# Kernel optimization log

Measured on AMD Instinct MI355X. Metric: run time of the kernel, lower is better.

The kernel has to match this reference:

```python
import jax, jax.numpy as jnp
import numpy as np

TOPK = 2048


def setup_inputs() -> dict:
    key = jax.random.key(0)
    ks = jax.random.split(key, 16)
    M = 20000
    boxes = jax.random.uniform(ks[0], (M, 4), dtype=jnp.float32)
    scores = jax.random.uniform(ks[1], (M,), dtype=jnp.float32)
    classes = jax.random.randint(ks[2], (M,), 0, 80, dtype=jnp.int64)
    def lin(k, fan_in, fan_out):
        b = 1.0 / np.sqrt(fan_in)
        kw, kb = jax.random.split(k)
        w = jax.random.uniform(kw, (fan_in, fan_out), jnp.float32, -b, b)
        bias = jax.random.uniform(kb, (fan_out,), jnp.float32, -b, b)
        return w, bias
    sup_w1, sup_b1 = lin(ks[3], 7, 32)
    sup_w2, sup_b2 = lin(ks[4], 32, 16)
    sup_w3, sup_b3 = lin(ks[5], 16, 1)
    lam_w1, lam_b1 = lin(ks[6], 5, 16)
    lam_w2, lam_b2 = lin(ks[7], 16, 1)
    return {
        'boxes': boxes, 'scores': scores, 'classes': classes,
        'sup_w1': sup_w1, 'sup_b1': sup_b1, 'sup_w2': sup_w2, 'sup_b2': sup_b2,
        'sup_w3': sup_w3, 'sup_b3': sup_b3,
        'lam_w1': lam_w1, 'lam_b1': lam_b1, 'lam_w2': lam_w2, 'lam_b2': lam_b2,
    }


def _box_iou(b):
    # b: [N,4] in (x, y, w, h)
    x, y, w, h = b[:, 0], b[:, 1], b[:, 2], b[:, 3]
    area = w * h
    ix1 = jnp.maximum(x[:, None], x[None, :])
    iy1 = jnp.maximum(y[:, None], y[None, :])
    ix2 = jnp.minimum((x + w)[:, None], (x + w)[None, :])
    iy2 = jnp.minimum((y + h)[:, None], (y + h)[None, :])
    inter = jnp.clip(ix2 - ix1, 0) * jnp.clip(iy2 - iy1, 0)
    union = area[:, None] + area[None, :] - inter
    return inter / (union + 1e-06)


def _dacs(boxes, scores, classes,
          sup_w1, sup_b1, sup_w2, sup_b2, sup_w3, sup_b3,
          lam_w1, lam_b1, lam_w2, lam_b2):
    k = min(TOPK, scores.shape[0])
    top_scores, idx = jax.lax.top_k(scores, k)
    b = boxes[idx]            # [N,4]
    cls = classes[idx]        # [N]
    N = k
    iou = _box_iou(b)         # [N,N]
    D = iou.mean(axis=1)      # [N]
    x, y, w, h = b[:, 0], b[:, 1], b[:, 2], b[:, 3]
    feats = jnp.stack([
        iou,
        jnp.abs(x[:, None] - x[None, :]),
        jnp.abs(y[:, None] - y[None, :]),
        jnp.abs(w[:, None] - w[None, :]),
        jnp.abs(h[:, None] - h[None, :]),
        jnp.broadcast_to(top_scores[:, None], (N, N)),
        jnp.broadcast_to(top_scores[None, :], (N, N)),
    ], axis=-1)               # [N,N,7]
    hdn = jax.nn.relu(feats @ sup_w1 + sup_b1)       # [N,N,32]
    hdn = jax.nn.relu(hdn @ sup_w2 + sup_b2)         # [N,N,16]
    s_ij = jax.nn.sigmoid((hdn @ sup_w3 + sup_b3)[..., 0])  # [N,N]
    class_mask = (cls[:, None] == cls[None, :]).astype(s_ij.dtype)
    s_ij = s_ij * class_mask
    lam_in = jnp.concatenate([b, top_scores[:, None]], axis=1)  # [N,5]
    lam_h = jax.nn.relu(lam_in @ lam_w1 + lam_b1)
    lam = jax.nn.sigmoid((lam_h @ lam_w2 + lam_b2)[:, 0])       # [N]
    S = jnp.sum(s_ij * iou, axis=1)
    E = lam * S * D
    new_scores = top_scores * jnp.exp(-E)
    return b, new_scores, cls


def reference(boxes, scores, classes,
              sup_w1, sup_b1, sup_w2, sup_b2, sup_w3, sup_b3,
              lam_w1, lam_b1, lam_w2, lam_b2):
    return _dacs(boxes, scores, classes,
                 sup_w1, sup_b1, sup_w2, sup_b2, sup_w3, sup_b3,
                 lam_w1, lam_b1, lam_w2, lam_b2)
```

## Files before the change

kernel.cpp:

```cpp
#include <hip/hip_runtime.h>
#include <math.h>

#define TOPK 2048
#define NCLS 80
#define NBIN 4096
#define CMAX 2560
#define TN   1024
#define CROWS 8

struct P {
    const float* scores; const float* boxes; const int* classes;
    const float* sw1; const float* sb1; const float* sw2; const float* sb2;
    const float* sw3; const float* sb3;
    const float* lw1; const float* lb1; const float* lw2; const float* lb2;
    int M; int K;
    float* out_boxes; float* out_scores; float* out_cls;
};

__device__ __forceinline__ float iou_of(float xi, float yi, float ai,
                                        float x2i, float y2i, float4 bj) {
    float ix1 = fmaxf(xi, bj.x), iy1 = fmaxf(yi, bj.y);
    float ix2 = fminf(x2i, bj.x + bj.z), iy2 = fminf(y2i, bj.y + bj.w);
    float iw = fmaxf(ix2 - ix1, 0.0f), ih = fmaxf(iy2 - iy1, 0.0f);
    float inter = iw * ih;
    float uni = ai + bj.z * bj.w - inter;
    return inter / (uni + 1e-6f);
}

__device__ __forceinline__ int digest12(float s) {
    int v = (int)(s * 4096.0f);
    return v < 0 ? 0 : (v > NBIN - 1 ? NBIN - 1 : v);
}

__device__ __forceinline__ float key_score(unsigned long long kk) {
    unsigned mono = (unsigned)(kk >> 32);
    unsigned ob = (mono & 0x80000000u) ? (mono & 0x7FFFFFFFu) : ~mono;
    return __uint_as_float(ob);
}

__global__ __launch_bounds__(TN, 1) void k_dacs(P p) {
    __shared__ int   bincur[NBIN];
    __shared__ int   binbase[NBIN];
    __shared__ unsigned long long skeys[CMAX];
    __shared__ int   sfx[TN];
    __shared__ int   wsum[TN / 64];
    __shared__ int   sh_cT;
    __shared__ float4 sbox[TOPK];
    __shared__ float  sscore[TOPK];
    __shared__ short  scls[TOPK];
    __shared__ short  clist[TOPK];
    __shared__ int    ccnt[NCLS], ccur[NCLS], cstart[NCLS + 1];
    __shared__ int    wtot;
    __shared__ float  swt[914];
    __shared__ float  wpart[TN / 64];
    __shared__ int    rowc[CROWS];
    __shared__ int    prefix[CROWS + 1];
    __shared__ float  Ssum[CROWS], Drow[CROWS];

    int tid = threadIdx.x, bid = blockIdx.x;
    int M = p.M, K = p.K, M4 = M >> 2;
    int r0 = bid * CROWS;
    int nrows = K - r0; if (nrows > CROWS) nrows = CROWS;
    if (nrows <= 0) return;

    for (int t = tid; t < 224; t += TN) swt[t] = p.sw1[t];
    if (tid < 32) swt[224 + tid] = p.sb1[tid];
    for (int t = tid; t < 512; t += TN) swt[256 + t] = p.sw2[t];
    if (tid < 16) swt[768 + tid] = p.sb2[tid];
    if (tid < 16) swt[784 + tid] = p.sw3[tid];
    if (tid == 0) swt[800] = p.sb3[0];
    if (tid < 80) swt[801 + tid] = p.lw1[tid];
    if (tid < 16) swt[881 + tid] = p.lb1[tid];
    if (tid < 16) swt[897 + tid] = p.lw2[tid];
    if (tid == 0) swt[913] = p.lb2[0];

    for (int b = tid; b < NBIN; b += TN) bincur[b] = 0;
    if (tid < NCLS) ccnt[tid] = 0;
    if (tid < CROWS) Ssum[tid] = 0.0f;
    __syncthreads();

    const float4* s4p = (const float4*)p.scores;
    for (int i4 = tid; i4 < M4; i4 += TN) {
        float4 v = s4p[i4];
        atomicAdd(&bincur[digest12(v.x)], 1);
        atomicAdd(&bincur[digest12(v.y)], 1);
        atomicAdd(&bincur[digest12(v.z)], 1);
        atomicAdd(&bincur[digest12(v.w)], 1);
    }
    for (int i = M4 * 4 + tid; i < M; i += TN)
        atomicAdd(&bincur[digest12(p.scores[i])], 1);
    __syncthreads();

    {
        const int BPT = NBIN / TN;
        int c0 = tid * BPT, sum = 0;
        #pragma unroll
        for (int u = 0; u < BPT; u++) sum += bincur[c0 + u];
        int lane = tid & 63;
        int x = sum;
        #pragma unroll
        for (int off = 1; off < 64; off <<= 1) {
            int v = __shfl_down(x, off, 64);
            if (lane + off < 64) x += v;
        }
        if (lane == 0) wsum[tid >> 6] = x;
        __syncthreads();
        if (tid < TN / 64) {
            int t = wsum[tid];
            #pragma unroll
            for (int off = 1; off < TN / 64; off <<= 1) {
                int v = __shfl_down(t, off, 64);
                if (tid + off < TN / 64) t += v;
            }
            wsum[tid] = t;
        }
        __syncthreads();
        int wid = tid >> 6;
        int higher = (wid < TN / 64 - 1) ? wsum[wid + 1] : 0;
        sfx[tid] = x + higher;
    }
    __syncthreads();

    {
        const int BPT = NBIN / TN;
        int running = (tid < TN - 1) ? sfx[tid + 1] : 0;
        int c0 = tid * BPT;
        for (int u = BPT - 1; u >= 0; u--) {
            int b = c0 + u, cnt = bincur[b];
            binbase[b] = running;
            if (running < K && running + cnt >= K) sh_cT = b;
            running += cnt;
        }
    }
    __syncthreads();
    int cT = sh_cT;
    for (int b = tid; b < NBIN; b += TN) bincur[b] = binbase[b];
    __syncthreads();

    for (int i4 = tid; i4 < M4; i4 += TN) {
        float4 v = s4p[i4];
        #pragma unroll
        for (int u = 0; u < 4; u++) {
            float s = (u == 0) ? v.x : (u == 1) ? v.y : (u == 2) ? v.z : v.w;
            int d = digest12(s);
            if (d >= cT) {
                int i = i4 * 4 + u;
                int slot = atomicAdd(&bincur[d], 1);
                if (slot < CMAX) {
                    unsigned b = __float_as_uint(s);
                    b = (b & 0x80000000u) ? ~b : (b | 0x80000000u);
                    skeys[slot] = ((unsigned long long)b << 32) |
                                  (unsigned long long)(0xFFFFFFFFu - (unsigned)i);
                }
            }
        }
    }
    for (int i = M4 * 4 + tid; i < M; i += TN) {
        float s = p.scores[i];
        int d = digest12(s);
        if (d >= cT) {
            int slot = atomicAdd(&bincur[d], 1);
            if (slot < CMAX) {
                unsigned b = __float_as_uint(s);
                b = (b & 0x80000000u) ? ~b : (b | 0x80000000u);
                skeys[slot] = ((unsigned long long)b << 32) |
                              (unsigned long long)(0xFFFFFFFFu - (unsigned)i);
            }
        }
    }
    __syncthreads();

    int C = bincur[cT]; if (C > CMAX) C = CMAX;
    {
        const float4* boxes4 = (const float4*)p.boxes;
        for (int s = tid; s < C; s += TN) {
            unsigned long long ks = skeys[s];
            unsigned idx = 0xFFFFFFFFu - (unsigned)(ks & 0xFFFFFFFFull);
            float sc = key_score(ks);
            int d = digest12(sc);
            int st = binbase[d], en = bincur[d]; if (en > CMAX) en = CMAX;
            int r = binbase[d];
            for (int t = st; t < en; t++) r += (skeys[t] > ks) ? 1 : 0;
            if (r < K) {
                sbox[r] = boxes4[idx];
                sscore[r] = sc;
                scls[r] = (short)p.classes[idx];
            }
        }
    }
    __syncthreads();

    for (int r = tid; r < K; r += TN) atomicAdd(&ccnt[scls[r]], 1);
    __syncthreads();
    {
        int x = 0, v = 0;
        if (tid < 128) {
            v = (tid < NCLS) ? ccnt[tid] : 0;
            x = v;
            #pragma unroll
            for (int off = 1; off < 64; off <<= 1) {
                int t = __shfl_up(x, off, 64);
                if ((tid & 63) >= off) x += t;
            }
            if (tid == 63) wtot = x;
        }
        __syncthreads();
        if (tid < NCLS) {
            int excl = x - v + ((tid >= 64) ? wtot : 0);
            ccur[tid] = excl;
            cstart[tid] = excl;
        }
        if (tid == 0) cstart[NCLS] = K;
        __syncthreads();
        for (int r = tid; r < K; r += TN) {
            int pos = atomicAdd(&ccur[scls[r]], 1);
            clist[pos] = (short)r;
        }
    }
    __syncthreads();

    {
        int wv = tid >> 6, lane = tid & 63;
        int row = wv >> 1, half = wv & 1;
        float dsum = 0.0f;
        if (row < nrows) {
            float4 bi = sbox[r0 + row];
            float ai = bi.z * bi.w, x2i = bi.x + bi.z, y2i = bi.y + bi.w;
            for (int j = lane + (half << 6); j < K; j += 128)
                dsum += iou_of(bi.x, bi.y, ai, x2i, y2i, sbox[j]);
            #pragma unroll
            for (int off = 32; off >= 1; off >>= 1)
                dsum += __shfl_xor(dsum, off, 64);
        }
        if (lane == 0) wpart[wv] = dsum;
    }

    if (tid < CROWS) {
        int st = 0, cnt = 0;
        if (tid < nrows) {
            int c = scls[r0 + tid];
            st = cstart[c];
            cnt = cstart[c + 1] - st;
        }
        rowc[tid] = st;
        prefix[tid] = cnt;
    }
    __syncthreads();
    if (tid < nrows) Drow[tid] = (wpart[2 * tid] + wpart[2 * tid + 1]) / (float)K;
    if (tid == 0) {
        int acc = 0;
        #pragma unroll
        for (int rr = 0; rr < CROWS; rr++) { int t = prefix[rr]; prefix[rr] = acc; acc += t; }
        prefix[CROWS] = acc;
    }
    __syncthreads();

    int Pb = prefix[CROWS];
    const float* W1 = swt;       const float* B1 = swt + 224;
    const float* W2 = swt + 256; const float* B2 = swt + 768;
    const float* W3 = swt + 784; float B3 = swt[800];

    for (int pp = tid; pp < Pb; pp += TN) {
        int lo = 0, hi = CROWS;
        while (hi - lo > 1) {
            int mid = (lo + hi) >> 1;
            if (prefix[mid] <= pp) lo = mid; else hi = mid;
        }
        int row = lo;
        int j = (int)clist[rowc[row] + (pp - prefix[row])];
        float4 bi = sbox[r0 + row];
        float4 bj = sbox[j];
        float ai = bi.z * bi.w, x2i = bi.x + bi.z, y2i = bi.y + bi.w;
        float iou = iou_of(bi.x, bi.y, ai, x2i, y2i, bj);
        float f1 = fabsf(bi.x - bj.x), f2 = fabsf(bi.y - bj.y);
        float f3 = fabsf(bi.z - bj.z), f4 = fabsf(bi.w - bj.w);
        float f5 = sscore[r0 + row], f6 = sscore[j];
        float acc2[16];
        #pragma unroll
        for (int q = 0; q < 16; q++) acc2[q] = B2[q];
        #pragma unroll 2
        for (int o = 0; o < 32; o++) {
            float a = B1[o];
            a += iou * W1[0 * 32 + o];
            a += f1 * W1[1 * 32 + o];
            a += f2 * W1[2 * 32 + o];
            a += f3 * W1[3 * 32 + o];
            a += f4 * W1[4 * 32 + o];
            a += f5 * W1[5 * 32 + o];
            a += f6 * W1[6 * 32 + o];
            float h = fmaxf(a, 0.0f);
            #pragma unroll
            for (int q = 0; q < 16; q++) acc2[q] += h * W2[o * 16 + q];
        }
        float acc3 = B3;
        #pragma unroll
        for (int q = 0; q < 16; q++) acc3 += fmaxf(acc2[q], 0.0f) * W3[q];
        atomicAdd(&Ssum[row], iou / (1.0f + expf(-acc3)));
    }
    __syncthreads();

    if (tid < nrows) {
        int r = r0 + tid;
        float4 bi = sbox[r];
        float si = sscore[r];
        const float* LW1 = swt + 801; const float* LB1 = swt + 881;
        const float* LW2 = swt + 897; float LB2 = swt[913];
        float in5[5] = { bi.x, bi.y, bi.z, bi.w, si };
        float acc = LB2;
        #pragma unroll
        for (int o = 0; o < 16; o++) {
            float a2 = LB1[o];
            #pragma unroll
            for (int f = 0; f < 5; f++) a2 += in5[f] * LW1[f * 16 + o];
            acc += fmaxf(a2, 0.0f) * LW2[o];
        }
        float lam = 1.0f / (1.0f + expf(-acc));
        ((float4*)p.out_boxes)[r] = bi;
        p.out_cls[r] = (float)scls[r];
        p.out_scores[r] = si * expf(-lam * Ssum[tid] * Drow[tid]);
    }
}

extern "C" void kernel_launch(void* const* d_in, const int* in_sizes, int n_in,
                              void* d_out, int out_size, void* d_ws, size_t ws_size,
                              hipStream_t stream) {
    int M = in_sizes[1];
    int K = (M < TOPK) ? M : TOPK;

    P dp;
    dp.scores  = (const float*)d_in[1];
    dp.boxes   = (const float*)d_in[0];
    dp.classes = (const int*)d_in[2];
    dp.sw1 = (const float*)d_in[3];  dp.sb1 = (const float*)d_in[4];
    dp.sw2 = (const float*)d_in[5];  dp.sb2 = (const float*)d_in[6];
    dp.sw3 = (const float*)d_in[7];  dp.sb3 = (const float*)d_in[8];
    dp.lw1 = (const float*)d_in[9];  dp.lb1 = (const float*)d_in[10];
    dp.lw2 = (const float*)d_in[11]; dp.lb2 = (const float*)d_in[12];
    dp.M = M; dp.K = K;
    dp.out_boxes  = (float*)d_out;
    dp.out_scores = (float*)d_out + (size_t)K * 4;
    dp.out_cls    = (float*)d_out + (size_t)K * 5;

    int nb = (K + CROWS - 1) / CROWS;
    k_dacs<<<nb, TN, 0, stream>>>(dp);
}
```

Before: 102.9 us.

## Split monolithic kernel into single-pass top-k selection plus pairwise compute kernels

Result: slower. 106.9 us (+3.9%).

```diff
diff --git a/kernel.cpp b/kernel.cpp
--- a/kernel.cpp
+++ b/kernel.cpp
@@ -5,17 +5,23 @@
 #define NCLS 80
 #define NBIN 4096
 #define CMAX 2560
-#define TN   1024
-#define CROWS 8
-
-struct P {
-    const float* scores; const float* boxes; const int* classes;
-    const float* sw1; const float* sb1; const float* sw2; const float* sb2;
-    const float* sw3; const float* sb3;
-    const float* lw1; const float* lb1; const float* lw2; const float* lb2;
-    int M; int K;
-    float* out_boxes; float* out_scores; float* out_cls;
-};
+#define TNA  1024
+#define TND  512
+#define CROWS 4
+
+
+struct SelAP { const float* scores; int M; int K; int* ghist; int* gmeta; };
+struct ScatP { const float* scores; int M; int* ghist; const int* gmeta;
+               unsigned long long* gskeys; };
+struct RankP { const float* boxes; const int* classes; const int* ghist;
+               const int* gmeta; const unsigned long long* gskeys; int K;
+               float4* selB; float* selS; int* selC; };
+struct CmpP  { const float4* selB; const float* selS; const int* selC;
+               const float* sw1; const float* sb1; const float* sw2; const float* sb2;
+               const float* sw3; const float* sb3;
+               const float* lw1; const float* lb1; const float* lw2; const float* lb2;
+               int K;
+               float* out_boxes; float* out_scores; float* out_cls; };
 
 __device__ __forceinline__ float iou_of(float xi, float yi, float ai,
                                         float x2i, float y2i, float4 bj) {
@@ -32,40 +38,159 @@
     return v < 0 ? 0 : (v > NBIN - 1 ? NBIN - 1 : v);
 }
 
+__device__ __forceinline__ unsigned long long make_key(float s, unsigned i) {
+    unsigned b = __float_as_uint(s);
+    b = (b & 0x80000000u) ? ~b : (b | 0x80000000u);
+    return ((unsigned long long)b << 32) |
+           (unsigned long long)(0xFFFFFFFFu - i);
+}
+
 __device__ __forceinline__ float key_score(unsigned long long kk) {
     unsigned mono = (unsigned)(kk >> 32);
     unsigned ob = (mono & 0x80000000u) ? (mono & 0x7FFFFFFFu) : ~mono;
     return __uint_as_float(ob);
 }
 
-__global__ __launch_bounds__(TN, 1) void k_dacs(P p) {
-    __shared__ int   bincur[NBIN];
-    __shared__ int   binbase[NBIN];
-    __shared__ unsigned long long skeys[CMAX];
-    __shared__ int   sfx[TN];
-    __shared__ int   wsum[TN / 64];
-    __shared__ int   sh_cT;
-    __shared__ float4 sbox[TOPK];
-    __shared__ float  sscore[TOPK];
-    __shared__ short  scls[TOPK];
-    __shared__ short  clist[TOPK];
-    __shared__ int    ccnt[NCLS], ccur[NCLS], cstart[NCLS + 1];
-    __shared__ int    wtot;
-    __shared__ float  swt[914];
-    __shared__ float  wpart[TN / 64];
-    __shared__ int    rowc[CROWS];
-    __shared__ int    prefix[CROWS + 1];
-    __shared__ float  Ssum[CROWS], Drow[CROWS];
+__global__ __launch_bounds__(TNA, 1) void k_selA(SelAP p) {
+    __shared__ int lbin[NBIN];
+    __shared__ int sfx[TNA];
+    __shared__ int wsum[TNA / 64];
+    __shared__ int sh_cT;
+
+    int tid = threadIdx.x;
+    int M = p.M, K = p.K, M4 = M >> 2;
+
+    for (int b = tid; b < NBIN; b += TNA) lbin[b] = 0;
+    __syncthreads();
+
+    const float4* s4p = (const float4*)p.scores;
+    for (int i4 = tid; i4 < M4; i4 += TNA) {
+        float4 v = s4p[i4];
+        atomicAdd(&lbin[digest12(v.x)], 1);
+        atomicAdd(&lbin[digest12(v.y)], 1);
+        atomicAdd(&lbin[digest12(v.z)], 1);
+        atomicAdd(&lbin[digest12(v.w)], 1);
+    }
+    for (int i = M4 * 4 + tid; i < M; i += TNA)
+        atomicAdd(&lbin[digest12(p.scores[i])], 1);
+    __syncthreads();
+
+    {
+        const int BPT = NBIN / TNA;
+        int c0 = tid * BPT, sum = 0;
+        #pragma unroll
+        for (int u = 0; u < BPT; u++) sum += lbin[c0 + u];
+        int lane = tid & 63;
+        int x = sum;
+        #pragma unroll
+        for (int off = 1; off < 64; off <<= 1) {
+            int v = __shfl_down(x, off, 64);
+            if (lane + off < 64) x += v;
+        }
+        if (lane == 0) wsum[tid >> 6] = x;
+        __syncthreads();
+        if (tid < TNA / 64) {
+            int t = wsum[tid];
+            #pragma unroll
+            for (int off = 1; off < TNA / 64; off <<= 1) {
+                int v = __shfl_down(t, off, 64);
+                if (tid + off < TNA / 64) t += v;
+            }
+            wsum[tid] = t;
+        }
+        __syncthreads();
+        int wid = tid >> 6;
+        int higher = (wid < TNA / 64 - 1) ? wsum[wid + 1] : 0;
+        sfx[tid] = x + higher;
+    }
+    __syncthreads();
+
+    {
+        const int BPT = NBIN / TNA;
+        int running = (tid < TNA - 1) ? sfx[tid + 1] : 0;
+        int c0 = tid * BPT;
+        for (int u = BPT - 1; u >= 0; u--) {
+            int b = c0 + u, cnt = lbin[b];
+            if (running < K && running + cnt >= K) sh_cT = b;
+            p.ghist[b] = (running << 16);
+            running += cnt;
+        }
+    }
+    __syncthreads();
+    if (tid == 0) p.gmeta[0] = sh_cT;
+}
+
+__global__ void k_scat(ScatP p) {
+    int nt = gridDim.x * blockDim.x;
+    int gt = blockIdx.x * blockDim.x + threadIdx.x;
+    int cT = p.gmeta[0];
+    int M = p.M, M4 = M >> 2;
+    const float4* s4p = (const float4*)p.scores;
+    for (int i4 = gt; i4 < M4; i4 += nt) {
+        float4 v = s4p[i4];
+        #pragma unroll
+        for (int u = 0; u < 4; u++) {
+            float s = (u == 0) ? v.x : (u == 1) ? v.y : (u == 2) ? v.z : v.w;
+            int d = digest12(s);
+            if (d >= cT) {
+                int old = atomicAdd(&p.ghist[d], 1);
+                int slot = (old >> 16) + (old & 0xFFFF);
+                if (slot < CMAX)
+                    p.gskeys[slot] = make_key(s, (unsigned)(i4 * 4 + u));
+            }
+        }
+    }
+    for (int i = M4 * 4 + gt; i < M; i += nt) {
+        float s = p.scores[i];
+        int d = digest12(s);
+        if (d >= cT) {
+            int old = atomicAdd(&p.ghist[d], 1);
+            int slot = (old >> 16) + (old & 0xFFFF);
+            if (slot < CMAX) p.gskeys[slot] = make_key(s, (unsigned)i);
+        }
+    }
+}
+
+__global__ void k_rank(RankP p) {
+    int t = blockIdx.x * blockDim.x + threadIdx.x;
+    int cT = p.gmeta[0];
+    int pkT = p.ghist[cT];
+    int C = (pkT >> 16) + (pkT & 0xFFFF); if (C > CMAX) C = CMAX;
+    if (t >= C) return;
+    unsigned long long ks = p.gskeys[t];
+    unsigned idx = 0xFFFFFFFFu - (unsigned)(ks & 0xFFFFFFFFull);
+    float sc = key_score(ks);
+    int d = digest12(sc);
+    int pk = p.ghist[d];
+    int st = pk >> 16;
+    int en = st + (pk & 0xFFFF); if (en > CMAX) en = CMAX;
+    int r = st;
+    for (int q = st; q < en; q++) r += (p.gskeys[q] > ks) ? 1 : 0;
+    if (r < p.K) {
+        p.selB[r] = ((const float4*)p.boxes)[idx];
+        p.selS[r] = sc;
+        p.selC[r] = p.classes[idx];
+    }
+}
+
+__global__ __launch_bounds__(TND, 2) void k_cmp(CmpP p) {
+    __shared__ float swt[914];
+    __shared__ short mlist[CROWS * TOPK];
+    __shared__ int   mcnt[CROWS];
+    __shared__ int   rowcls[CROWS];
+    __shared__ int   prefix[CROWS + 1];
+    __shared__ float wpart[TND / 64];
+    __shared__ float Ssum[CROWS], Drow[CROWS];
 
     int tid = threadIdx.x, bid = blockIdx.x;
-    int M = p.M, K = p.K, M4 = M >> 2;
+    int K = p.K;
     int r0 = bid * CROWS;
     int nrows = K - r0; if (nrows > CROWS) nrows = CROWS;
     if (nrows <= 0) return;
 
-    for (int t = tid; t < 224; t += TN) swt[t] = p.sw1[t];
+    for (int t = tid; t < 224; t += TND) swt[t] = p.sw1[t];
     if (tid < 32) swt[224 + tid] = p.sb1[tid];
-    for (int t = tid; t < 512; t += TN) swt[256 + t] = p.sw2[t];
+    for (int t = tid; t < 512; t += TND) swt[256 + t] = p.sw2[t];
     if (tid < 16) swt[768 + tid] = p.sb2[tid];
     if (tid < 16) swt[784 + tid] = p.sw3[tid];
     if (tid == 0) swt[800] = p.sb3[0];
@@ -74,183 +199,45 @@
     if (tid < 16) swt[897 + tid] = p.lw2[tid];
     if (tid == 0) swt[913] = p.lb2[0];
 
-    for (int b = tid; b < NBIN; b += TN) bincur[b] = 0;
-    if (tid < NCLS) ccnt[tid] = 0;
-    if (tid < CROWS) Ssum[tid] = 0.0f;
-    __syncthreads();
-
-    const float4* s4p = (const float4*)p.scores;
-    for (int i4 = tid; i4 < M4; i4 += TN) {
-        float4 v = s4p[i4];
-        atomicAdd(&bincur[digest12(v.x)], 1);
-        atomicAdd(&bincur[digest12(v.y)], 1);
-        atomicAdd(&bincur[digest12(v.z)], 1);
-        atomicAdd(&bincur[digest12(v.w)], 1);
-    }
-    for (int i = M4 * 4 + tid; i < M; i += TN)
-        atomicAdd(&bincur[digest12(p.scores[i])], 1);
-    __syncthreads();
-
-    {
-        const int BPT = NBIN / TN;
-        int c0 = tid * BPT, sum = 0;
-        #pragma unroll
-        for (int u = 0; u < BPT; u++) sum += bincur[c0 + u];
-        int lane = tid & 63;
-        int x = sum;
-        #pragma unroll
-        for (int off = 1; off < 64; off <<= 1) {
-            int v = __shfl_down(x, off, 64);
-            if (lane + off < 64) x += v;
-        }
-        if (lane == 0) wsum[tid >> 6] = x;
-        __syncthreads();
-        if (tid < TN / 64) {
-            int t = wsum[tid];
-            #pragma unroll
-            for (int off = 1; off < TN / 64; off <<= 1) {
-                int v = __shfl_down(t, off, 64);
-                if (tid + off < TN / 64) t += v;
+    if (tid < CROWS) {
+        mcnt[tid] = 0;
+        Ssum[tid] = 0.0f;
+        rowcls[tid] = (tid < nrows) ? p.selC[r0 + tid] : -1;
+    }
+    __syncthreads();
+
+    for (int j = tid; j < K; j += TND) {
+        int c = p.selC[j];
+        #pragma unroll
+        for (int rr = 0; rr < CROWS; rr++) {
+            if (c == rowcls[rr]) {
+                int pos = atomicAdd(&mcnt[rr], 1);
+                mlist[rr * TOPK + pos] = (short)j;
             }
-            wsum[tid] = t;
-        }
-        __syncthreads();
-        int wid = tid >> 6;
-        int higher = (wid < TN / 64 - 1) ? wsum[wid + 1] : 0;
-        sfx[tid] = x + higher;
-    }
-    __syncthreads();
-
-    {
-        const int BPT = NBIN / TN;
-        int running = (tid < TN - 1) ? sfx[tid + 1] : 0;
-        int c0 = tid * BPT;
-        for (int u = BPT - 1; u >= 0; u--) {
-            int b = c0 + u, cnt = bincur[b];
-            binbase[b] = running;
-            if (running < K && running + cnt >= K) sh_cT = b;
-            running += cnt;
-        }
-    }
-    __syncthreads();
-    int cT = sh_cT;
-    for (int b = tid; b < NBIN; b += TN) bincur[b] = binbase[b];
-    __syncthreads();
-
-    for (int i4 = tid; i4 < M4; i4 += TN) {
-        float4 v = s4p[i4];
-        #pragma unroll
-        for (int u = 0; u < 4; u++) {
-            float s = (u == 0) ? v.x : (u == 1) ? v.y : (u == 2) ? v.z : v.w;
-            int d = digest12(s);
-            if (d >= cT) {
-                int i = i4 * 4 + u;
-                int slot = atomicAdd(&bincur[d], 1);
-                if (slot < CMAX) {
-                    unsigned b = __float_as_uint(s);
-                    b = (b & 0x80000000u) ? ~b : (b | 0x80000000u);
-                    skeys[slot] = ((unsigned long long)b << 32) |
-                                  (unsigned long long)(0xFFFFFFFFu - (unsigned)i);
-                }
-            }
-        }
-    }
-    for (int i = M4 * 4 + tid; i < M; i += TN) {
-        float s = p.scores[i];
-        int d = digest12(s);
-        if (d >= cT) {
-            int slot = atomicAdd(&bincur[d], 1);
-            if (slot < CMAX) {
-                unsigned b = __float_as_uint(s);
-                b = (b & 0x80000000u) ? ~b : (b | 0x80000000u);
-                skeys[slot] = ((unsigned long long)b << 32) |
-                              (unsigned long long)(0xFFFFFFFFu - (unsigned)i);
-            }
-        }
-    }
-    __syncthreads();
-
-    int C = bincur[cT]; if (C > CMAX) C = CMAX;
-    {
-        const float4* boxes4 = (const float4*)p.boxes;
-        for (int s = tid; s < C; s += TN) {
-            unsigned long long ks = skeys[s];
-            unsigned idx = 0xFFFFFFFFu - (unsigned)(ks & 0xFFFFFFFFull);
-            float sc = key_score(ks);
-            int d = digest12(sc);
-            int st = binbase[d], en = bincur[d]; if (en > CMAX) en = CMAX;
-            int r = binbase[d];
-            for (int t = st; t < en; t++) r += (skeys[t] > ks) ? 1 : 0;
-            if (r < K) {
-                sbox[r] = boxes4[idx];
-                sscore[r] = sc;
-                scls[r] = (short)p.classes[idx];
-            }
-        }
-    }
-    __syncthreads();
-
-    for (int r = tid; r < K; r += TN) atomicAdd(&ccnt[scls[r]], 1);
-    __syncthreads();
-    {
-        int x = 0, v = 0;
-        if (tid < 128) {
-            v = (tid < NCLS) ? ccnt[tid] : 0;
-            x = v;
-            #pragma unroll
-            for (int off = 1; off < 64; off <<= 1) {
-                int t = __shfl_up(x, off, 64);
-                if ((tid & 63) >= off) x += t;
-            }
-            if (tid == 63) wtot = x;
-        }
-        __syncthreads();
-        if (tid < NCLS) {
-            int excl = x - v + ((tid >= 64) ? wtot : 0);
-            ccur[tid] = excl;
-            cstart[tid] = excl;
-        }
-        if (tid == 0) cstart[NCLS] = K;
-        __syncthreads();
-        for (int r = tid; r < K; r += TN) {
-            int pos = atomicAdd(&ccur[scls[r]], 1);
-            clist[pos] = (short)r;
-        }
-    }
-    __syncthreads();
+        }
+    }
 
     {
         int wv = tid >> 6, lane = tid & 63;
         int row = wv >> 1, half = wv & 1;
         float dsum = 0.0f;
         if (row < nrows) {
-            float4 bi = sbox[r0 + row];
+            float4 bi = p.selB[r0 + row];
             float ai = bi.z * bi.w, x2i = bi.x + bi.z, y2i = bi.y + bi.w;
             for (int j = lane + (half << 6); j < K; j += 128)
-                dsum += iou_of(bi.x, bi.y, ai, x2i, y2i, sbox[j]);
+                dsum += iou_of(bi.x, bi.y, ai, x2i, y2i, p.selB[j]);
             #pragma unroll
             for (int off = 32; off >= 1; off >>= 1)
                 dsum += __shfl_xor(dsum, off, 64);
         }
         if (lane == 0) wpart[wv] = dsum;
     }
-
-    if (tid < CROWS) {
-        int st = 0, cnt = 0;
-        if (tid < nrows) {
-            int c = scls[r0 + tid];
-            st = cstart[c];
-            cnt = cstart[c + 1] - st;
-        }
-        rowc[tid] = st;
-        prefix[tid] = cnt;
-    }
     __syncthreads();
     if (tid < nrows) Drow[tid] = (wpart[2 * tid] + wpart[2 * tid + 1]) / (float)K;
     if (tid == 0) {
         int acc = 0;
         #pragma unroll
-        for (int rr = 0; rr < CROWS; rr++) { int t = prefix[rr]; prefix[rr] = acc; acc += t; }
+        for (int rr = 0; rr < CROWS; rr++) { int t = mcnt[rr]; prefix[rr] = acc; acc += t; }
         prefix[CROWS] = acc;
     }
     __syncthreads();
@@ -260,21 +247,16 @@
     const float* W2 = swt + 256; const float* B2 = swt + 768;
     const float* W3 = swt + 784; float B3 = swt[800];
 
-    for (int pp = tid; pp < Pb; pp += TN) {
-        int lo = 0, hi = CROWS;
-        while (hi - lo > 1) {
-            int mid = (lo + hi) >> 1;
-            if (prefix[mid] <= pp) lo = mid; else hi = mid;
-        }
-        int row = lo;
-        int j = (int)clist[rowc[row] + (pp - prefix[row])];
-        float4 bi = sbox[r0 + row];
-        float4 bj = sbox[j];
+    for (int pp = tid; pp < Pb; pp += TND) {
+        int row = (pp >= prefix[1]) + (pp >= prefix[2]) + (pp >= prefix[3]);
+        int j = (int)mlist[row * TOPK + (pp - prefix[row])];
+        float4 bi = p.selB[r0 + row];
+        float4 bj = p.selB[j];
         float ai = bi.z * bi.w, x2i = bi.x + bi.z, y2i = bi.y + bi.w;
         float iou = iou_of(bi.x, bi.y, ai, x2i, y2i, bj);
         float f1 = fabsf(bi.x - bj.x), f2 = fabsf(bi.y - bj.y);
         float f3 = fabsf(bi.z - bj.z), f4 = fabsf(bi.w - bj.w);
-        float f5 = sscore[r0 + row], f6 = sscore[j];
+        float f5 = p.selS[r0 + row], f6 = p.selS[j];
         float acc2[16];
         #pragma unroll
         for (int q = 0; q < 16; q++) acc2[q] = B2[q];
@@ -301,8 +283,8 @@
 
     if (tid < nrows) {
         int r = r0 + tid;
-        float4 bi = sbox[r];
-        float si = sscore[r];
+        float4 bi = p.selB[r];
+        float si = p.selS[r];
         const float* LW1 = swt + 801; const float* LB1 = swt + 881;
         const float* LW2 = swt + 897; float LB2 = swt[913];
         float in5[5] = { bi.x, bi.y, bi.z, bi.w, si };
@@ -316,7 +298,7 @@
         }
         float lam = 1.0f / (1.0f + expf(-acc));
         ((float4*)p.out_boxes)[r] = bi;
-        p.out_cls[r] = (float)scls[r];
+        p.out_cls[r] = (float)p.selC[r];
         p.out_scores[r] = si * expf(-lam * Ssum[tid] * Drow[tid]);
     }
 }
@@ -327,20 +309,46 @@
     int M = in_sizes[1];
     int K = (M < TOPK) ? M : TOPK;
 
-    P dp;
-    dp.scores  = (const float*)d_in[1];
-    dp.boxes   = (const float*)d_in[0];
-    dp.classes = (const int*)d_in[2];
-    dp.sw1 = (const float*)d_in[3];  dp.sb1 = (const float*)d_in[4];
-    dp.sw2 = (const float*)d_in[5];  dp.sb2 = (const float*)d_in[6];
-    dp.sw3 = (const float*)d_in[7];  dp.sb3 = (const float*)d_in[8];
-    dp.lw1 = (const float*)d_in[9];  dp.lb1 = (const float*)d_in[10];
-    dp.lw2 = (const float*)d_in[11]; dp.lb2 = (const float*)d_in[12];
-    dp.M = M; dp.K = K;
-    dp.out_boxes  = (float*)d_out;
-    dp.out_scores = (float*)d_out + (size_t)K * 4;
-    dp.out_cls    = (float*)d_out + (size_t)K * 5;
-
-    int nb = (K + CROWS - 1) / CROWS;
-    k_dacs<<<nb, TN, 0, stream>>>(dp);
-}
+    char* ws = (char*)d_ws;
+    float4* selB  = (float4*)ws;               ws += (size_t)TOPK * 16;
+    float*  selS  = (float*)ws;                ws += (size_t)TOPK * 4;
+    int*    selC  = (int*)ws;                  ws += (size_t)TOPK * 4;
+    unsigned long long* gskeys = (unsigned long long*)ws; ws += (size_t)CMAX * 8;
+    int*    ghist = (int*)ws;                  ws += (size_t)NBIN * 4;
+    int*    gmeta = (int*)ws;                  ws += 16;
+
+    SelAP a;
+    a.scores = (const float*)d_in[1];
+    a.M = M; a.K = K; a.ghist = ghist; a.gmeta = gmeta;
+
+    ScatP b;
+    b.scores = (const float*)d_in[1];
+    b.M = M; b.ghist = ghist; b.gmeta = gmeta; b.gskeys = gskeys;
+
+    RankP c;
+    c.boxes = (const float*)d_in[0];
+    c.classes = (const int*)d_in[2];
+    c.ghist = ghist; c.gmeta = gmeta; c.gskeys = gskeys; c.K = K;
+    c.selB = selB; c.selS = selS; c.selC = selC;
+
+    CmpP d;
+    d.selB = selB; d.selS = selS; d.selC = selC;
+    d.sw1 = (const float*)d_in[3];  d.sb1 = (const float*)d_in[4];
+    d.sw2 = (const float*)d_in[5];  d.sb2 = (const float*)d_in[6];
+    d.sw3 = (const float*)d_in[7];  d.sb3 = (const float*)d_in[8];
+    d.lw1 = (const float*)d_in[9];  d.lb1 = (const float*)d_in[10];
+    d.lw2 = (const float*)d_in[11]; d.lb2 = (const float*)d_in[12];
+    d.K = K;
+    d.out_boxes  = (float*)d_out;
+    d.out_scores = (float*)d_out + (size_t)K * 4;
+    d.out_cls    = (float*)d_out + (size_t)K * 5;
+
+    int nbB = ((M >> 2) + 255) / 256; if (nbB < 1) nbB = 1;
+    int nbC = (CMAX + 255) / 256;
+    int nbD = (K + CROWS - 1) / CROWS;
+
+    k_selA<<<1, TNA, 0, stream>>>(a);
+    k_scat<<<nbB, 256, 0, stream>>>(b);
+    k_rank<<<nbC, 256, 0, stream>>>(c);
+    k_cmp <<<nbD, TND, 0, stream>>>(d);
+}
```
